# Optimization experiments

Measured on AMD Instinct MI355X. Metric: run time of the kernel, lower is better.

The kernel has to match this reference:

```python
import jax, jax.numpy as jnp
import numpy as np
from jax import lax

DN = ('NCDHW', 'OIDHW', 'NCDHW')
BN_EPS = 1e-5
COS_EPS = 1e-8   # torch CosineSimilarity eps
L1_EPS = 1e-12   # F.normalize default eps


def _lrelu(x):
    return jnp.where(x >= 0, x, 0.2 * x)


def _bn(x, g, b):
    # BatchNorm3d in training mode: batch statistics over (N, D, H, W)
    m = jnp.mean(x, axis=(0, 2, 3, 4), keepdims=True)
    v = jnp.var(x, axis=(0, 2, 3, 4), keepdims=True)
    return g[None, :, None, None, None] * (x - m) * lax.rsqrt(v + BN_EPS) + b[None, :, None, None, None]


def _conv(x, w, b, stride):
    y = lax.conv_general_dilated(x, w, window_strides=stride, padding=[(1, 1)] * 3,
                                 dimension_numbers=DN)
    return y + b[None, :, None, None, None]


def _convT(x, w, b, stride, out_pad):
    # ConvTranspose3d(k=3, padding=1, output_padding=out_pad) == input-dilated conv
    # with flipped kernel and padding (k-1-p, k-1-p+op) = (1, 1+op).
    k = jnp.flip(w, axis=(2, 3, 4))
    y = lax.conv_general_dilated(x, k, window_strides=(1, 1, 1),
                                 padding=[(1, 1 + o) for o in out_pad],
                                 lhs_dilation=stride, dimension_numbers=DN)
    return y + b[None, :, None, None, None]


def setup_inputs() -> dict:
    key = jax.random.key(0)
    ks = jax.random.split(key, 20)
    d = {}
    d['x'] = jax.random.normal(ks[0], (2, 1, 16, 256, 256), jnp.float32)
    enc = [(96, 1), (128, 96), (256, 128), (256, 256)]
    for i, (co, ci) in enumerate(enc):
        fan = ci * 27
        d[f'enc_w{i+1}'] = jax.random.normal(ks[1 + i], (co, ci, 3, 3, 3), jnp.float32) * np.float32(np.sqrt(2.0 / fan))
        d[f'enc_b{i+1}'] = jnp.zeros((co,), jnp.float32)
        d[f'enc_g{i+1}'] = jnp.ones((co,), jnp.float32)
        d[f'enc_be{i+1}'] = jnp.zeros((co,), jnp.float32)
    d['mem'] = jax.random.normal(ks[5], (2000, 256), jnp.float32) * np.float32(1.0 / np.sqrt(256))
    dec = [(256, 256), (128, 256), (96, 128), (1, 96)]  # (Cout, Cin)
    for i, (co, ci) in enumerate(dec):
        fan = ci * 27
        d[f'dec_w{i+1}'] = jax.random.normal(ks[6 + i], (co, ci, 3, 3, 3), jnp.float32) * np.float32(np.sqrt(2.0 / fan))
        d[f'dec_b{i+1}'] = jnp.zeros((co,), jnp.float32)
        if i < 3:
            d[f'dec_g{i+1}'] = jnp.ones((co,), jnp.float32)
            d[f'dec_be{i+1}'] = jnp.zeros((co,), jnp.float32)
    return d


def _forward(x,
             enc_w1, enc_b1, enc_g1, enc_be1,
             enc_w2, enc_b2, enc_g2, enc_be2,
             enc_w3, enc_b3, enc_g3, enc_be3,
             enc_w4, enc_b4, enc_g4, enc_be4,
             mem,
             dec_w1, dec_b1, dec_g1, dec_be1,
             dec_w2, dec_b2, dec_g2, dec_be2,
             dec_w3, dec_b3, dec_g3, dec_be3,
             dec_w4, dec_b4):
    # ---- encoder ----
    f = _lrelu(_bn(_conv(x, enc_w1, enc_b1, (1, 2, 2)), enc_g1, enc_be1))
    f = _lrelu(_bn(_conv(f, enc_w2, enc_b2, (2, 2, 2)), enc_g2, enc_be2))
    f = _lrelu(_bn(_conv(f, enc_w3, enc_b3, (2, 2, 2)), enc_g3, enc_be3))
    f = _lrelu(_bn(_conv(f, enc_w4, enc_b4, (2, 2, 2)), enc_g4, enc_be4))
    # ---- memory addressing (cosine similarity without materializing repeats) ----
    N, C, D, H, W = f.shape
    z = f.transpose(0, 2, 3, 4, 1).reshape(-1, C)                    # [M, C]
    z_norm = jnp.linalg.norm(z, axis=1, keepdims=True)               # [M, 1]
    m_norm = jnp.linalg.norm(mem, axis=1, keepdims=True)             # [K, 1]
    num = z @ mem.T                                                  # [M, K]
    den = jnp.maximum(z_norm * m_norm.T, COS_EPS)
    w = jax.nn.softmax(num / den, axis=1)
    w_hat = jax.nn.relu(w)
    w_hat = w_hat / jnp.maximum(jnp.sum(jnp.abs(w_hat), axis=1, keepdims=True), L1_EPS)
    z_hat = w_hat @ mem                                              # [M, C]
    zf = z_hat.reshape(N, D, H, W, C).transpose(0, 4, 1, 2, 3)
    # ---- decoder ----
    y = _lrelu(_bn(_convT(zf, dec_w1, dec_b1, (2, 2, 2), (1, 1, 1)), dec_g1, dec_be1))
    y = _lrelu(_bn(_convT(y, dec_w2, dec_b2, (2, 2, 2), (1, 1, 1)), dec_g2, dec_be2))
    y = _lrelu(_bn(_convT(y, dec_w3, dec_b3, (2, 2, 2), (1, 1, 1)), dec_g3, dec_be3))
    out = _convT(y, dec_w4, dec_b4, (1, 2, 2), (0, 1, 1))
    return out, w_hat


def reference(x,
              enc_w1, enc_b1, enc_g1, enc_be1,
              enc_w2, enc_b2, enc_g2, enc_be2,
              enc_w3, enc_b3, enc_g3, enc_be3,
              enc_w4, enc_b4, enc_g4, enc_be4,
              mem,
              dec_w1, dec_b1, dec_g1, dec_be1,
              dec_w2, dec_b2, dec_g2, dec_be2,
              dec_w3, dec_b3, dec_g3, dec_be3,
              dec_w4, dec_b4):
    return _forward(x,
                    enc_w1, enc_b1, enc_g1, enc_be1,
                    enc_w2, enc_b2, enc_g2, enc_be2,
                    enc_w3, enc_b3, enc_g3, enc_be3,
                    enc_w4, enc_b4, enc_g4, enc_be4,
                    mem,
                    dec_w1, dec_b1, dec_g1, dec_be1,
                    dec_w2, dec_b2, dec_g2, dec_be2,
                    dec_w3, dec_b3, dec_g3, dec_be3,
                    dec_w4, dec_b4)
```

## Files before the change

### kernel.cpp

```cpp
#include <hip/hip_runtime.h>
#include <math.h>

typedef unsigned short u16;
typedef __bf16 bf16;
typedef bf16 bf16x8 __attribute__((ext_vector_type(8)));
typedef float f32x4 __attribute__((ext_vector_type(4)));
typedef u16 u16x8 __attribute__((ext_vector_type(8)));

__device__ inline float b2f(u16 u){ unsigned x = ((unsigned)u) << 16; return __builtin_bit_cast(float, x); }
__device__ inline u16 f2b(float f){ bf16 b = (bf16)f; return __builtin_bit_cast(u16, b); }
__device__ inline f32x4 mfma16(bf16x8 a, bf16x8 b, f32x4 c){
    return __builtin_amdgcn_mfma_f32_16x16x32_bf16(a, b, c, 0, 0, 0);
}
__device__ inline void unp8(uint4 v, float* f){
    f[0]=__builtin_bit_cast(float, v.x<<16); f[1]=__builtin_bit_cast(float, v.x&0xffff0000u);
    f[2]=__builtin_bit_cast(float, v.y<<16); f[3]=__builtin_bit_cast(float, v.y&0xffff0000u);
    f[4]=__builtin_bit_cast(float, v.z<<16); f[5]=__builtin_bit_cast(float, v.z&0xffff0000u);
    f[6]=__builtin_bit_cast(float, v.w<<16); f[7]=__builtin_bit_cast(float, v.w&0xffff0000u);
}

struct Rep7 {
    const float* src[7];
    u16* dst[7];
    int co[7];
    int ci[7];
};
__global__ __launch_bounds__(256) void repack7_k(Rep7 a)
{
    int w = blockIdx.y;
    const float* src = a.src[w]; u16* dst = a.dst[w];
    int Co = a.co[w], Ci = a.ci[w];
    int tot = 27 * Co * Ci;
    for (int e = blockIdx.x * 256 + threadIdx.x; e < tot; e += gridDim.x * 256) {
        int ci = e % Ci; int t2 = e / Ci; int co = t2 % Co; int tp = t2 / Co;
        dst[e] = f2b(src[(size_t)(co * Ci + ci) * 27 + tp]);
    }
}

template<bool ISCONV, int CK, int BN>
__global__ __launch_bounds__(512) void conv_mfma3_k(
    const u16* __restrict__ in, const u16* __restrict__ wt,
    const float* __restrict__ bias, u16* __restrict__ out,
    float* __restrict__ pm, float* __restrict__ pv,
    int Ci, int Co, int Di, int Hi, int Wi,
    int ld, int lh, int lw, int Do, int Ho, int Wo)
{
    constexpr int NK = CK / 32;
    constexpr int NF = BN / 32;
    __shared__ u16 As[128][CK + 8];
    __shared__ u16 Bs[BN][CK + 8];
    const int tid = threadIdx.x;
    const int mtile = blockIdx.x, co0 = blockIdx.y * BN;
    int pd = 0, ph = 0, pw = 0;
    if (!ISCONV) { int bz = blockIdx.z; pd = bz >> 2; ph = (bz >> 1) & 1; pw = bz & 1; }

    const int arow = tid >> 2, seg = tid & 3;
    int xo, yo, zo, n;
    { int m = mtile * 128 + arow;
      xo = m & ((1 << lw) - 1); m >>= lw;
      yo = m & ((1 << lh) - 1); m >>= lh;
      zo = m & ((1 << ld) - 1); n = m >> ld; }
    const bool isb = arow < BN;

    const int wave = tid >> 6, lane = tid & 63;
    const int wm = wave >> 1, wn = wave & 1;
    const int fr = lane & 15, fs = lane >> 4;

    f32x4 acc[2][NF];
    #pragma unroll
    for (int mf = 0; mf < 2; ++mf)
        #pragma unroll
        for (int nf = 0; nf < NF; ++nf) acc[mf][nf] = f32x4{0,0,0,0};

    const int ntd = ISCONV ? 3 : pd + 1;
    const int nth = ISCONV ? 3 : ph + 1;
    const int ntw = ISCONV ? 3 : pw + 1;
    const size_t HiWi = (size_t)Hi * Wi;

    for (int jd = 0; jd < ntd; ++jd) {
        int zi = ISCONV ? 2 * zo + jd - 1 : zo + (pd ? jd : 0);
        int wd = ISCONV ? jd : (pd ? (jd ? 0 : 2) : 1);
        bool vz = (unsigned)zi < (unsigned)Di;
        for (int jh = 0; jh < nth; ++jh) {
            int yi = ISCONV ? 2 * yo + jh - 1 : yo + (ph ? jh : 0);
            int wh = ISCONV ? jh : (ph ? (jh ? 0 : 2) : 1);
            bool vy = vz && ((unsigned)yi < (unsigned)Hi);
            for (int jw = 0; jw < ntw; ++jw) {
                int xi = ISCONV ? 2 * xo + jw - 1 : xo + (pw ? jw : 0);
                int ww = ISCONV ? jw : (pw ? (jw ? 0 : 2) : 1);
                bool va = vy && ((unsigned)xi < (unsigned)Wi);
                size_t abase = 0;
                if (va) abase = (((size_t)(n * Di + zi)) * HiWi + (size_t)yi * Wi + xi) * Ci;
                int widx = wd * 9 + wh * 3 + ww;
                size_t bbase = ((size_t)widx * Co + (co0 + arow)) * (size_t)Ci;
                for (int ck = 0; ck < Ci; ck += CK) {
                    uint4 av[NK], bv[NK];
                    #pragma unroll
                    for (int k = 0; k < NK; ++k) {
                        int col = ck + k * 32 + seg * 8;
                        av[k] = va  ? *reinterpret_cast<const uint4*>(in + abase + col) : uint4{0,0,0,0};
                        bv[k] = isb ? *reinterpret_cast<const uint4*>(wt + bbase + col) : uint4{0,0,0,0};
                    }
                    __syncthreads();
                    #pragma unroll
                    for (int k = 0; k < NK; ++k) {
                        *reinterpret_cast<uint4*>(&As[arow][k * 32 + seg * 8]) = av[k];
                        if (isb) *reinterpret_cast<uint4*>(&Bs[arow][k * 32 + seg * 8]) = bv[k];
                    }
                    __syncthreads();
                    #pragma unroll
                    for (int k = 0; k < NK; ++k) {
                        bf16x8 a0 = *reinterpret_cast<const bf16x8*>(&As[wm * 32      + fr][k * 32 + fs * 8]);
                        bf16x8 a1 = *reinterpret_cast<const bf16x8*>(&As[wm * 32 + 16 + fr][k * 32 + fs * 8]);
                        #pragma unroll
                        for (int nf = 0; nf < NF; ++nf) {
                            bf16x8 b = *reinterpret_cast<const bf16x8*>(
                                &Bs[wn * (BN / 2) + nf * 16 + fr][k * 32 + fs * 8]);
                            acc[0][nf] = mfma16(a0, b, acc[0][nf]);
                            acc[1][nf] = mfma16(a1, b, acc[1][nf]);
                        }
                    }
                }
            }
        }
    }
    float bi[NF], s[NF], q[NF];
    #pragma unroll
    for (int nf = 0; nf < NF; ++nf) {
        bi[nf] = bias[co0 + wn * (BN / 2) + nf * 16 + fr];
        s[nf] = 0.f; q[nf] = 0.f;
    }
    #pragma unroll
    for (int mf = 0; mf < 2; ++mf) {
        #pragma unroll
        for (int j = 0; j < 4; ++j) {
            int rm = mtile * 128 + wm * 32 + mf * 16 + fs * 4 + j;
            size_t vox;
            if (ISCONV) vox = (size_t)rm;
            else {
                int X = rm & ((1 << lw) - 1); int m2 = rm >> lw;
                int Y = m2 & ((1 << lh) - 1); m2 >>= lh;
                int Z = m2 & ((1 << ld) - 1); int nn = m2 >> ld;
                vox = (((size_t)(nn * Do + (2 * Z + pd))) * Ho + (2 * Y + ph)) * Wo + (2 * X + pw);
            }
            #pragma unroll
            for (int nf = 0; nf < NF; ++nf) {
                float f = acc[mf][nf][j] + bi[nf];
                out[vox * Co + (co0 + wn * (BN / 2) + nf * 16 + fr)] = f2b(f);
                s[nf] += f; q[nf] += f * f;
            }
        }
    }
    __syncthreads();
    float* bnS = reinterpret_cast<float*>(&As[0][0]);
    float* bnQ = bnS + BN * 16;
    #pragma unroll
    for (int nf = 0; nf < NF; ++nf) {
        int cl = wn * (BN / 2) + nf * 16 + fr;
        bnS[cl * 16 + wm * 4 + fs] = s[nf];
        bnQ[cl * 16 + wm * 4 + fs] = q[nf];
    }
    __syncthreads();
    if (tid < BN) {
        float S = 0.f, Q = 0.f;
        #pragma unroll
        for (int i = 0; i < 16; ++i) { S += bnS[tid * 16 + i]; Q += bnQ[tid * 16 + i]; }
        int p = blockIdx.x + gridDim.x * (blockIdx.y + gridDim.y * blockIdx.z);
        pm[(size_t)p * BN + tid] = S;
        pv[(size_t)p * BN + tid] = Q;
    }
}

__global__ __launch_bounds__(256) void enc1_k(
    const float* __restrict__ x, const float* __restrict__ w,
    const float* __restrict__ bias, u16* __restrict__ out)
{
    __shared__ float Xi[4 * 17 * 33];
    __shared__ float Wl[96 * 27];
    __shared__ float Bl[96];
    const int tid = threadIdx.x;
    int t = blockIdx.x;
    const int tx = t & 7; t >>= 3;
    const int ty = t & 15; t >>= 4;
    const int tz = t;
    const int n = blockIdx.y;
    const int z0 = tz * 2, y0 = ty * 8, x0 = tx * 16;
    for (int i = tid; i < 2592; i += 256) Wl[i] = w[i];
    for (int i = tid; i < 96; i += 256) Bl[i] = bias[i];
    for (int i = tid; i < 2244; i += 256) {
        int fz = i / 561; int r = i - fz * 561; int fy = r / 33; int fx = r - fy * 33;
        int zi = z0 - 1 + fz, yi = 2 * y0 - 1 + fy, xi = 2 * x0 - 1 + fx;
        float v = 0.f;
        if ((unsigned)zi < 16u && (unsigned)yi < 256u && (unsigned)xi < 256u)
            v = x[((size_t)(n * 16 + zi) * 256 + yi) * 256 + xi];
        Xi[i] = v;
    }
    __syncthreads();
    const int lx = tid & 15, ly = (tid >> 4) & 7, lz = tid >> 7;
    float iv[27];
    #pragma unroll
    for (int kd = 0; kd < 3; ++kd)
        #pragma unroll
        for (int kh = 0; kh < 3; ++kh)
            #pragma unroll
            for (int kw = 0; kw < 3; ++kw)
                iv[kd * 9 + kh * 3 + kw] = Xi[(lz + kd) * 561 + (2 * ly + kh) * 33 + (2 * lx + kw)];
    size_t vox = ((size_t)(n * 16 + z0 + lz) * 128 + (y0 + ly)) * 128 + (x0 + lx);
    u16* op = out + vox * 96;
    #pragma unroll
    for (int og = 0; og < 12; ++og) {
        u16x8 pk;
        #pragma unroll
        for (int oo = 0; oo < 8; ++oo) {
            int o = og * 8 + oo;
            float a = Bl[o];
            #pragma unroll
            for (int tp = 0; tp < 27; ++tp) a += iv[tp] * Wl[o * 27 + tp];
            pk[oo] = f2b(a);
        }
        *reinterpret_cast<u16x8*>(op + og * 8) = pk;
    }
}

__global__ __launch_bounds__(256) void dec4g_k(
    const u16* __restrict__ in, const u16* __restrict__ wt4,
    float* __restrict__ P)
{
    __shared__ u16 As[64][120];
    __shared__ u16 Bs[32][120];
    const int tid = threadIdx.x;
    const int vox0 = blockIdx.x << 6;
    for (int i = tid; i < 384; i += 256) {
        int row = i / 12, seg = i - row * 12;
        uint4 v = {0,0,0,0};
        if (row < 27) v = *reinterpret_cast<const uint4*>(wt4 + row * 96 + seg * 8);
        *reinterpret_cast<uint4*>(&Bs[row][seg * 8]) = v;
    }
    for (int i = tid; i < 768; i += 256) {
        int row = i / 12, seg = i - row * 12;
        uint4 v = *reinterpret_cast<const uint4*>(in + (size_t)(vox0 + row) * 96 + seg * 8);
        *reinterpret_cast<uint4*>(&As[row][seg * 8]) = v;
    }
    __syncthreads();
    const int wave = tid >> 6, lane = tid & 63;
    const int fr = lane & 15, fs = lane >> 4;
    f32x4 acc0 = {0,0,0,0}, acc1 = {0,0,0,0};
    #pragma unroll
    for (int kk = 0; kk < 3; ++kk) {
        bf16x8 a  = *reinterpret_cast<const bf16x8*>(&As[wave * 16 + fr][kk * 32 + fs * 8]);
        bf16x8 b0 = *reinterpret_cast<const bf16x8*>(&Bs[fr     ][kk * 32 + fs * 8]);
        bf16x8 b1 = *reinterpret_cast<const bf16x8*>(&Bs[16 + fr][kk * 32 + fs * 8]);
        acc0 = mfma16(a, b0, acc0);
        acc1 = mfma16(a, b1, acc1);
    }
    #pragma unroll
    for (int j = 0; j < 4; ++j) {
        int vox = vox0 + wave * 16 + fs * 4 + j;
        P[(size_t)vox * 32 + fr]      = acc0[j];
        P[(size_t)vox * 32 + 16 + fr] = acc1[j];
    }
}

__global__ __launch_bounds__(256) void dec4s_k(
    const float* __restrict__ P, const float* __restrict__ bias,
    float* __restrict__ out)
{
    __shared__ float Pl[180 * 33];
    const int tid = threadIdx.x;
    int b = blockIdx.x;
    const int tx = b & 15; b >>= 4;
    const int ty = b & 31; b >>= 5;
    const int tz = b;
    const int n = blockIdx.y;
    const int Z0 = tz * 2, Y0 = ty * 8, X0 = tx * 16;
    const int yi0 = Y0 >> 1, xi0 = X0 >> 1;
    for (int i = tid; i < 5760; i += 256) {
        int row = i >> 5, c = i & 31;
        int dz = row / 45; int r = row - dz * 45; int dy = r / 9; int dx = r - dy * 9;
        int zi = Z0 - 1 + dz, yi = yi0 + dy, xi = xi0 + dx;
        float v = 0.f;
        if (zi >= 0 && zi < 16 && yi < 128 && xi < 128)
            v = P[((size_t)((n * 16 + zi) * 128 + yi) * 128 + xi) * 32 + c];
        Pl[row * 33 + c] = v;
    }
    __syncthreads();
    const int lx = tid & 15, ly = (tid >> 4) & 7, lz = tid >> 7;
    float acc = bias[0];
    #pragma unroll
    for (int qd = 0; qd < 3; ++qd) {
        int t = Z0 + lz + qd - 1;
        if (t < 0 || t >= 16) continue;
        int dz = lz + qd;
        #pragma unroll
        for (int qh = 0; qh < 3; ++qh) {
            int u = ly + qh - 1;
            if (u & 1) continue;
            int dy = u >> 1;
            #pragma unroll
            for (int qw = 0; qw < 3; ++qw) {
                int v = lx + qw - 1;
                if (v & 1) continue;
                int dx = v >> 1;
                int widx = (2 - qd) * 9 + (2 - qh) * 3 + (2 - qw);
                acc += Pl[(dz * 45 + dy * 9 + dx) * 33 + widx];
            }
        }
    }
    out[((size_t)(n * 16 + Z0 + lz) * 256 + (Y0 + ly)) * 256 + (X0 + lx)] = acc;
}

__global__ __launch_bounds__(256) void bnstat_k(
    const u16* __restrict__ a, float* __restrict__ pm, float* __restrict__ pv,
    int C, unsigned total8)
{
    __shared__ float sS[256][8];
    __shared__ float sQ[256][8];
    unsigned g = blockIdx.x * 256 + threadIdx.x;
    unsigned stride = gridDim.x * 256;
    float s[8] = {0,0,0,0,0,0,0,0}, q[8] = {0,0,0,0,0,0,0,0};
    for (unsigned i = g; i < total8; i += stride) {
        uint4 v = *reinterpret_cast<const uint4*>(a + (size_t)i * 8);
        float f[8]; unp8(v, f);
        #pragma unroll
        for (int e = 0; e < 8; ++e) { s[e] += f[e]; q[e] += f[e] * f[e]; }
    }
    #pragma unroll
    for (int e = 0; e < 8; ++e) { sS[threadIdx.x][e] = s[e]; sQ[threadIdx.x][e] = q[e]; }
    __syncthreads();
    int c = threadIdx.x;
    if (c < C) {
        int C8 = C >> 3;
        int B = (int)((blockIdx.x * 2048u) % (unsigned)C);
        int r = c - B; r %= C; if (r < 0) r += C;
        int e = r & 7, t0 = r >> 3;
        float S = 0.f, Q = 0.f;
        for (int tt = t0; tt < 256; tt += C8) { S += sS[tt][e]; Q += sQ[tt][e]; }
        pm[blockIdx.x * C + c] = S;
        pv[blockIdx.x * C + c] = Q;
    }
}

__global__ __launch_bounds__(64) void bnfin_k(
    const float* __restrict__ pm, const float* __restrict__ pv,
    const float* __restrict__ g, const float* __restrict__ be,
    float* __restrict__ sc, float* __restrict__ sb, int C, int G, float invcnt)
{
    int c = blockIdx.x;
    float S = 0.f, Q = 0.f;
    for (int b = threadIdx.x; b < G; b += 64) { S += pm[b * C + c]; Q += pv[b * C + c]; }
    #pragma unroll
    for (int off = 32; off; off >>= 1) {
        S += __shfl_down(S, off, 64);
        Q += __shfl_down(Q, off, 64);
    }
    if (threadIdx.x == 0) {
        float m = S * invcnt;
        float v = Q * invcnt - m * m;
        float s = g[c] * rsqrtf(v + 1e-5f);
        sc[c] = s; sb[c] = be[c] - m * s;
    }
}

__global__ __launch_bounds__(64) void bnfin3_k(
    const float* __restrict__ pm, const float* __restrict__ pv,
    const float* __restrict__ g, const float* __restrict__ be,
    float* __restrict__ sc, float* __restrict__ sb,
    int C, int BNl, int gx, int gy, int gz, float invcnt)
{
    int c = blockIdx.x;
    int cog = c / BNl, cl = c % BNl;
    int tot = gx * gz;
    float S = 0.f, Q = 0.f;
    for (int i = threadIdx.x; i < tot; i += 64) {
        int bx = i % gx, bz = i / gx;
        int p = bx + gx * (cog + gy * bz);
        S += pm[(size_t)p * BNl + cl];
        Q += pv[(size_t)p * BNl + cl];
    }
    #pragma unroll
    for (int off = 32; off; off >>= 1) {
        S += __shfl_down(S, off, 64);
        Q += __shfl_down(Q, off, 64);
    }
    if (threadIdx.x == 0) {
        float m = S * invcnt;
        float v = Q * invcnt - m * m;
        float s = g[c] * rsqrtf(v + 1e-5f);
        sc[c] = s; sb[c] = be[c] - m * s;
    }
}

__global__ __launch_bounds__(256) void bnapply_k(
    u16* __restrict__ a, const float* __restrict__ sc, const float* __restrict__ sb,
    int C, unsigned total8)
{
    unsigned g = blockIdx.x * 256 + threadIdx.x;
    unsigned stride = gridDim.x * 256;
    int c0 = (int)((g * 8u) % (unsigned)C);
    float lsc[8], lsb[8];
    #pragma unroll
    for (int e = 0; e < 8; ++e) { lsc[e] = sc[c0 + e]; lsb[e] = sb[c0 + e]; }
    for (unsigned i = g; i < total8; i += stride) {
        uint4 v = *reinterpret_cast<const uint4*>(a + (size_t)i * 8);
        float f[8]; unp8(v, f);
        u16x8 pk;
        #pragma unroll
        for (int e = 0; e < 8; ++e) {
            float y = f[e] * lsc[e] + lsb[e];
            y = y >= 0.f ? y : 0.2f * y;
            pk[e] = f2b(y);
        }
        *reinterpret_cast<u16x8*>(a + (size_t)i * 8) = pk;
    }
}

__global__ __launch_bounds__(256) void memprep_k(
    const float* __restrict__ mem, u16* __restrict__ memb, u16* __restrict__ memT,
    float* __restrict__ mnorm)
{
    int k = blockIdx.x, c = threadIdx.x;
    if (k >= 2000) { memT[(size_t)c * 2048 + k] = 0; return; }
    float v = mem[(size_t)k * 256 + c];
    u16 b = f2b(v);
    memb[(size_t)k * 256 + c] = b;
    memT[(size_t)c * 2048 + k] = b;
    float s = v * v;
    #pragma unroll
    for (int off = 32; off; off >>= 1) s += __shfl_down(s, off, 64);
    __shared__ float red[4];
    if ((c & 63) == 0) red[c >> 6] = s;
    __syncthreads();
    if (c == 0) mnorm[k] = sqrtf(red[0] + red[1] + red[2] + red[3]);
}

__global__ __launch_bounds__(64) void znorm_k(
    const u16* __restrict__ z, float* __restrict__ znorm)
{
    int m = blockIdx.x, l = threadIdx.x;
    ushort4 v = *reinterpret_cast<const ushort4*>(z + (size_t)m * 256 + l * 4);
    float a = b2f(v.x), b = b2f(v.y), cc = b2f(v.z), d = b2f(v.w);
    float s = a * a + b * b + cc * cc + d * d;
    #pragma unroll
    for (int off = 32; off; off >>= 1) s += __shfl_down(s, off, 64);
    if (l == 0) znorm[m] = sqrtf(s);
}

__global__ __launch_bounds__(256) void scores_mfma_k(
    const u16* __restrict__ z, const u16* __restrict__ memb,
    const float* __restrict__ znorm, const float* __restrict__ mnorm,
    float* __restrict__ scores)
{
    __shared__ u16 As[64][40];
    __shared__ u16 Bs[64][40];
    const int tid = threadIdx.x;
    const int m0 = blockIdx.x << 6, n0 = blockIdx.y << 6;
    const int arow = tid >> 2, seg = tid & 3;
    const bool bok = (n0 + arow) < 2000;
    const int wave = tid >> 6, lane = tid & 63;
    const int wm = wave >> 1, wn = wave & 1, fr = lane & 15, fs = lane >> 4;
    f32x4 acc00 = {0,0,0,0}, acc01 = {0,0,0,0}, acc10 = {0,0,0,0}, acc11 = {0,0,0,0};
    for (int k0 = 0; k0 < 256; k0 += 32) {
        uint4 avv = *reinterpret_cast<const uint4*>(z + (size_t)(m0 + arow) * 256 + k0 + seg * 8);
        uint4 bvv = {0,0,0,0};
        if (bok) bvv = *reinterpret_cast<const uint4*>(memb + (size_t)(n0 + arow) * 256 + k0 + seg * 8);
        __syncthreads();
        *reinterpret_cast<uint4*>(&As[arow][seg * 8]) = avv;
        *reinterpret_cast<uint4*>(&Bs[arow][seg * 8]) = bvv;
        __syncthreads();
        bf16x8 a0 = *reinterpret_cast<const bf16x8*>(&As[wm * 32      + fr][fs * 8]);
        bf16x8 a1 = *reinterpret_cast<const bf16x8*>(&As[wm * 32 + 16 + fr][fs * 8]);
        bf16x8 b0 = *reinterpret_cast<const bf16x8*>(&Bs[wn * 32      + fr][fs * 8]);
        bf16x8 b1 = *reinterpret_cast<const bf16x8*>(&Bs[wn * 32 + 16 + fr][fs * 8]);
        acc00 = mfma16(a0, b0, acc00);
        acc01 = mfma16(a0, b1, acc01);
        acc10 = mfma16(a1, b0, acc10);
        acc11 = mfma16(a1, b1, acc11);
    }
    const int c0 = n0 + wn * 32 + fr, c1 = c0 + 16;
    float mn0 = (c0 < 2000) ? mnorm[c0] : 1.f;
    float mn1 = (c1 < 2000) ? mnorm[c1] : 1.f;
    #pragma unroll
    for (int mi = 0; mi < 2; ++mi) {
        f32x4 aN0 = mi ? acc10 : acc00;
        f32x4 aN1 = mi ? acc11 : acc01;
        #pragma unroll
        for (int j = 0; j < 4; ++j) {
            int rm = m0 + wm * 32 + mi * 16 + fs * 4 + j;
            float zn = znorm[rm];
            if (c0 < 2000) scores[(size_t)rm * 2000 + c0] = aN0[j] / fmaxf(zn * mn0, 1e-8f);
            if (c1 < 2000) scores[(size_t)rm * 2000 + c1] = aN1[j] / fmaxf(zn * mn1, 1e-8f);
        }
    }
}

__global__ __launch_bounds__(256) void softmax2_k(
    float* __restrict__ w, u16* __restrict__ wb16)
{
    __shared__ float red[4];
    const int m = blockIdx.x, t = threadIdx.x;
    const bool act = t < 250;
    float v[8];
    if (act) {
        float4 p0 = *reinterpret_cast<const float4*>(w + (size_t)m * 2000 + t * 8);
        float4 p1 = *reinterpret_cast<const float4*>(w + (size_t)m * 2000 + t * 8 + 4);
        v[0]=p0.x; v[1]=p0.y; v[2]=p0.z; v[3]=p0.w;
        v[4]=p1.x; v[5]=p1.y; v[6]=p1.z; v[7]=p1.w;
    } else {
        for (int i = 0; i < 8; ++i) v[i] = -1e30f;
    }
    float mx = -1e30f;
    for (int i = 0; i < 8; ++i) mx = fmaxf(mx, v[i]);
    #pragma unroll
    for (int off = 32; off; off >>= 1) mx = fmaxf(mx, __shfl_down(mx, off, 64));
    if ((t & 63) == 0) red[t >> 6] = mx;
    __syncthreads();
    mx = fmaxf(fmaxf(red[0], red[1]), fmaxf(red[2], red[3]));
    __syncthreads();
    float e[8], sm = 0.f;
    for (int i = 0; i < 8; ++i) {
        e[i] = act ? expf(v[i] - mx) : 0.f;
        sm += e[i];
    }
    #pragma unroll
    for (int off = 32; off; off >>= 1) sm += __shfl_down(sm, off, 64);
    if ((t & 63) == 0) red[t >> 6] = sm;
    __syncthreads();
    float inv = 1.0f / (red[0] + red[1] + red[2] + red[3]);
    u16x8 pk = {0,0,0,0,0,0,0,0};
    if (act) {
        float r[8];
        for (int i = 0; i < 8; ++i) { r[i] = e[i] * inv; pk[i] = f2b(r[i]); }
        float4 o0, o1;
        o0.x=r[0]; o0.y=r[1]; o0.z=r[2]; o0.w=r[3];
        o1.x=r[4]; o1.y=r[5]; o1.z=r[6]; o1.w=r[7];
        *reinterpret_cast<float4*>(w + (size_t)m * 2000 + t * 8)     = o0;
        *reinterpret_cast<float4*>(w + (size_t)m * 2000 + t * 8 + 4) = o1;
    }
    *reinterpret_cast<u16x8*>(wb16 + (size_t)m * 2048 + t * 8) = pk;
}

__global__ __launch_bounds__(256) void zhat_mfma_k(
    const u16* __restrict__ wb16, const u16* __restrict__ memT,
    u16* __restrict__ zf)
{
    __shared__ u16 As[64][40];
    __shared__ u16 Bs[64][40];
    const int tid = threadIdx.x;
    const int m0 = blockIdx.x << 6, n0 = blockIdx.y << 6;
    const int arow = tid >> 2, seg = tid & 3;
    const int wave = tid >> 6, lane = tid & 63;
    const int wm = wave >> 1, wn = wave & 1, fr = lane & 15, fs = lane >> 4;
    f32x4 acc00 = {0,0,0,0}, acc01 = {0,0,0,0}, acc10 = {0,0,0,0}, acc11 = {0,0,0,0};
    for (int k0 = 0; k0 < 2048; k0 += 32) {
        uint4 avv = *reinterpret_cast<const uint4*>(wb16 + (size_t)(m0 + arow) * 2048 + k0 + seg * 8);
        uint4 bvv = *reinterpret_cast<const uint4*>(memT + (size_t)(n0 + arow) * 2048 + k0 + seg * 8);
        __syncthreads();
        *reinterpret_cast<uint4*>(&As[arow][seg * 8]) = avv;
        *reinterpret_cast<uint4*>(&Bs[arow][seg * 8]) = bvv;
        __syncthreads();
        bf16x8 a0 = *reinterpret_cast<const bf16x8*>(&As[wm * 32      + fr][fs * 8]);
        bf16x8 a1 = *reinterpret_cast<const bf16x8*>(&As[wm * 32 + 16 + fr][fs * 8]);
        bf16x8 b0 = *reinterpret_cast<const bf16x8*>(&Bs[wn * 32      + fr][fs * 8]);
        bf16x8 b1 = *reinterpret_cast<const bf16x8*>(&Bs[wn * 32 + 16 + fr][fs * 8]);
        acc00 = mfma16(a0, b0, acc00);
        acc01 = mfma16(a0, b1, acc01);
        acc10 = mfma16(a1, b0, acc10);
        acc11 = mfma16(a1, b1, acc11);
    }
    const int c0 = n0 + wn * 32 + fr, c1 = c0 + 16;
    #pragma unroll
    for (int mi = 0; mi < 2; ++mi) {
        f32x4 aN0 = mi ? acc10 : acc00;
        f32x4 aN1 = mi ? acc11 : acc01;
        #pragma unroll
        for (int j = 0; j < 4; ++j) {
            int rm = m0 + wm * 32 + mi * 16 + fs * 4 + j;
            zf[(size_t)rm * 256 + c0] = f2b(aN0[j]);
            zf[(size_t)rm * 256 + c1] = f2b(aN1[j]);
        }
    }
}

extern "C" void kernel_launch(void* const* d_in, const int* in_sizes, int n_in,
                              void* d_out, int out_size, void* d_ws, size_t ws_size,
                              hipStream_t stream)
{
    const float* x     = (const float*)d_in[0];
    const float* ew[4] = { (const float*)d_in[1],  (const float*)d_in[5],
                           (const float*)d_in[9],  (const float*)d_in[13] };
    const float* eb[4] = { (const float*)d_in[2],  (const float*)d_in[6],
                           (const float*)d_in[10], (const float*)d_in[14] };
    const float* eg[4] = { (const float*)d_in[3],  (const float*)d_in[7],
                           (const float*)d_in[11], (const float*)d_in[15] };
    const float* ebe[4]= { (const float*)d_in[4],  (const float*)d_in[8],
                           (const float*)d_in[12], (const float*)d_in[16] };
    const float* mem   = (const float*)d_in[17];
    const float* dw[4] = { (const float*)d_in[18], (const float*)d_in[22],
                           (const float*)d_in[26], (const float*)d_in[30] };
    const float* db[4] = { (const float*)d_in[19], (const float*)d_in[23],
                           (const float*)d_in[27], (const float*)d_in[31] };
    const float* dg[3] = { (const float*)d_in[20], (const float*)d_in[24],
                           (const float*)d_in[28] };
    const float* dbe[3]= { (const float*)d_in[21], (const float*)d_in[25],
                           (const float*)d_in[29] };

    float* outp  = (float*)d_out;
    float* w_out = (float*)d_out + 2097152;

    char* p = (char*)d_ws;
    auto take = [&](size_t bytes) -> char* {
        char* q = p; p += (bytes + 255) & ~(size_t)255; return q;
    };
    u16* b1   = (u16*)take(50331648ull * 2);
    u16* b2   = (u16*)take(8388608ull * 2);
    u16* b3   = (u16*)take(2097152ull * 2);
    u16* b4   = (u16*)take(262144ull * 2);
    u16* zf   = (u16*)take(262144ull * 2);
    u16* w2   = (u16*)take(331776ull * 2);
    u16* w3   = (u16*)take(884736ull * 2);
    u16* w4   = (u16*)take(1769472ull * 2);
    u16* wd1  = (u16*)take(1769472ull * 2);
    u16* wd2  = (u16*)take(884736ull * 2);
    u16* wd3  = (u16*)take(331776ull * 2);
    u16* wd4  = (u16*)take(2592ull * 2);
    u16* memb = (u16*)take(512000ull * 2);
    u16* memT = (u16*)take(524288ull * 2);
    u16* wb16 = (u16*)take(2097152ull * 2);
    float* P     = (float*)take(16777216ull * 4);
    float* pm    = (float*)take(1048576ull * 4);
    float* pv    = (float*)take(1048576ull * 4);
    float* scb   = (float*)take(512 * 4);
    float* mnorm = (float*)take(2048 * 4);
    float* znorm = (float*)take(1024 * 4);

    auto bnc = [&](u16* buf, const float* g, const float* be, int C, int BNl,
                   unsigned total8, int G, int gx, int gy, int gz) {
        bnfin3_k<<<C, 64, 0, stream>>>(pm, pv, g, be, scb, scb + 256,
                                       C, BNl, gx, gy, gz,
                                       (float)C / ((float)total8 * 8.0f));
        bnapply_k<<<G, 256, 0, stream>>>(buf, scb, scb + 256, C, total8);
    };

    Rep7 ra;
    ra.src[0]=ew[1]; ra.dst[0]=w2;  ra.co[0]=128; ra.ci[0]=96;
    ra.src[1]=ew[2]; ra.dst[1]=w3;  ra.co[1]=256; ra.ci[1]=128;
    ra.src[2]=ew[3]; ra.dst[2]=w4;  ra.co[2]=256; ra.ci[2]=256;
    ra.src[3]=dw[0]; ra.dst[3]=wd1; ra.co[3]=256; ra.ci[3]=256;
    ra.src[4]=dw[1]; ra.dst[4]=wd2; ra.co[4]=128; ra.ci[4]=256;
    ra.src[5]=dw[2]; ra.dst[5]=wd3; ra.co[5]=96;  ra.ci[5]=128;
    ra.src[6]=dw[3]; ra.dst[6]=wd4; ra.co[6]=1;   ra.ci[6]=96;
    repack7_k<<<dim3(64, 7), 256, 0, stream>>>(ra);
    memprep_k<<<2048, 256, 0, stream>>>(mem, memb, memT, mnorm);

    enc1_k<<<dim3(1024, 2), 256, 0, stream>>>(x, ew[0], eb[0], b1);
    bnstat_k<<<768, 256, 0, stream>>>(b1, pm, pv, 96, 6291456u);
    bnfin_k<<<96, 64, 0, stream>>>(pm, pv, eg[0], ebe[0], scb, scb + 256, 96, 768,
                                   96.0f / (6291456.0f * 8.0f));
    bnapply_k<<<768, 256, 0, stream>>>(b1, scb, scb + 256, 96, 6291456u);

    conv_mfma3_k<true, 96, 128><<<dim3(512, 1, 1), 512, 0, stream>>>(
        b1, w2, eb[1], b2, pm, pv, 96, 128, 16, 128, 128, 3, 6, 6, 8, 64, 64);
    bnc(b2, eg[1], ebe[1], 128, 128, 1048576u, 512, 512, 1, 1);

    conv_mfma3_k<true, 128, 64><<<dim3(64, 4, 1), 512, 0, stream>>>(
        b2, w3, eb[2], b3, pm, pv, 128, 256, 8, 64, 64, 2, 5, 5, 4, 32, 32);
    bnc(b3, eg[2], ebe[2], 256, 64, 262144u, 512, 64, 4, 1);

    conv_mfma3_k<true, 128, 64><<<dim3(8, 4, 1), 512, 0, stream>>>(
        b3, w4, eb[3], b4, pm, pv, 256, 256, 4, 32, 32, 1, 4, 4, 2, 16, 16);
    bnc(b4, eg[3], ebe[3], 256, 64, 32768u, 128, 8, 4, 1);

    znorm_k<<<1024, 64, 0, stream>>>(b4, znorm);
    scores_mfma_k<<<dim3(16, 32), 256, 0, stream>>>(b4, memb, znorm, mnorm, w_out);
    softmax2_k<<<1024, 256, 0, stream>>>(w_out, wb16);
    zhat_mfma_k<<<dim3(16, 4), 256, 0, stream>>>(wb16, memT, zf);

    conv_mfma3_k<false, 128, 64><<<dim3(8, 4, 8), 512, 0, stream>>>(
        zf, wd1, db[0], b3, pm, pv, 256, 256, 2, 16, 16, 1, 4, 4, 4, 32, 32);
    bnc(b3, dg[0], dbe[0], 256, 64, 262144u, 512, 8, 4, 8);

    conv_mfma3_k<false, 128, 64><<<dim3(64, 2, 8), 512, 0, stream>>>(
        b3, wd2, db[1], b2, pm, pv, 256, 128, 4, 32, 32, 2, 5, 5, 8, 64, 64);
    bnc(b2, dg[1], dbe[1], 128, 64, 1048576u, 512, 64, 2, 8);

    conv_mfma3_k<false, 128, 96><<<dim3(512, 1, 8), 512, 0, stream>>>(
        b2, wd3, db[2], b1, pm, pv, 128, 96, 8, 64, 64, 3, 6, 6, 16, 128, 128);
    bnc(b1, dg[2], dbe[2], 96, 96, 6291456u, 768, 512, 1, 8);

    dec4g_k<<<8192, 256, 0, stream>>>(b1, wd4, P);
    dec4s_k<<<dim3(4096, 2), 256, 0, stream>>>(P, db[3], outp);
}
```

Before: 779.8 us.

## Fuse final BN+LeakyReLU into dec4 GEMM load; stage enc1 output stores via LDS

```diff
diff --git a/kernel.cpp b/kernel.cpp
--- a/kernel.cpp
+++ b/kernel.cpp
@@ -175,9 +175,8 @@
     const float* __restrict__ x, const float* __restrict__ w,
     const float* __restrict__ bias, u16* __restrict__ out)
 {
-    __shared__ float Xi[4 * 17 * 33];
-    __shared__ float Wl[96 * 27];
-    __shared__ float Bl[96];
+    __shared__ uint4 smem[256 * 13];
+    float* Xi = reinterpret_cast<float*>(smem);
     const int tid = threadIdx.x;
     int t = blockIdx.x;
     const int tx = t & 7; t >>= 3;
@@ -185,8 +184,6 @@
     const int tz = t;
     const int n = blockIdx.y;
     const int z0 = tz * 2, y0 = ty * 8, x0 = tx * 16;
-    for (int i = tid; i < 2592; i += 256) Wl[i] = w[i];
-    for (int i = tid; i < 96; i += 256) Bl[i] = bias[i];
     for (int i = tid; i < 2244; i += 256) {
         int fz = i / 561; int r = i - fz * 561; int fy = r / 33; int fx = r - fy * 33;
         int zi = z0 - 1 + fz, yi = 2 * y0 - 1 + fy, xi = 2 * x0 - 1 + fx;
@@ -205,25 +202,36 @@
             #pragma unroll
             for (int kw = 0; kw < 3; ++kw)
                 iv[kd * 9 + kh * 3 + kw] = Xi[(lz + kd) * 561 + (2 * ly + kh) * 33 + (2 * lx + kw)];
-    size_t vox = ((size_t)(n * 16 + z0 + lz) * 128 + (y0 + ly)) * 128 + (x0 + lx);
-    u16* op = out + vox * 96;
+    __syncthreads();
     #pragma unroll
     for (int og = 0; og < 12; ++og) {
         u16x8 pk;
         #pragma unroll
         for (int oo = 0; oo < 8; ++oo) {
             int o = og * 8 + oo;
-            float a = Bl[o];
+            float a = bias[o];
             #pragma unroll
-            for (int tp = 0; tp < 27; ++tp) a += iv[tp] * Wl[o * 27 + tp];
+            for (int tp = 0; tp < 27; ++tp) a += iv[tp] * w[o * 27 + tp];
             pk[oo] = f2b(a);
         }
-        *reinterpret_cast<u16x8*>(op + og * 8) = pk;
+        smem[tid * 13 + og] = __builtin_bit_cast(uint4, pk);
+    }
+    __syncthreads();
+    #pragma unroll
+    for (int it = 0; it < 12; ++it) {
+        int i = it * 256 + tid;
+        int r = i / 192, j = i - r * 192;
+        int rz = r >> 3, ry = r & 7;
+        int v = r * 16 + j / 12, c8 = j % 12;
+        uint4 val = smem[v * 13 + c8];
+        size_t voxbase = ((size_t)(n * 16 + z0 + rz) * 128 + (y0 + ry)) * 128 + x0;
+        *reinterpret_cast<uint4*>(out + voxbase * 96 + (size_t)j * 8) = val;
     }
 }
 
 __global__ __launch_bounds__(256) void dec4g_k(
     const u16* __restrict__ in, const u16* __restrict__ wt4,
+    const float* __restrict__ sc, const float* __restrict__ sb,
     float* __restrict__ P)
 {
     __shared__ u16 As[64][120];
@@ -239,7 +247,16 @@
     for (int i = tid; i < 768; i += 256) {
         int row = i / 12, seg = i - row * 12;
         uint4 v = *reinterpret_cast<const uint4*>(in + (size_t)(vox0 + row) * 96 + seg * 8);
-        *reinterpret_cast<uint4*>(&As[row][seg * 8]) = v;
+        float f[8]; unp8(v, f);
+        int c0 = seg * 8;
+        u16x8 pk;
+        #pragma unroll
+        for (int e = 0; e < 8; ++e) {
+            float y = f[e] * sc[c0 + e] + sb[c0 + e];
+            y = y >= 0.f ? y : 0.2f * y;
+            pk[e] = f2b(y);
+        }
+        *reinterpret_cast<u16x8*>(&As[row][seg * 8]) = pk;
     }
     __syncthreads();
     const int wave = tid >> 6, lane = tid & 63;
@@ -634,11 +651,11 @@
     float* znorm = (float*)take(1024 * 4);
 
     auto bnc = [&](u16* buf, const float* g, const float* be, int C, int BNl,
-                   unsigned total8, int G, int gx, int gy, int gz) {
+                   unsigned total8, int G, int gx, int gy, int gz, bool apply) {
         bnfin3_k<<<C, 64, 0, stream>>>(pm, pv, g, be, scb, scb + 256,
                                        C, BNl, gx, gy, gz,
                                        (float)C / ((float)total8 * 8.0f));
-        bnapply_k<<<G, 256, 0, stream>>>(buf, scb, scb + 256, C, total8);
+        if (apply) bnapply_k<<<G, 256, 0, stream>>>(buf, scb, scb + 256, C, total8);
     };
 
     Rep7 ra;
@@ -660,15 +677,15 @@
 
     conv_mfma3_k<true, 96, 128><<<dim3(512, 1, 1), 512, 0, stream>>>(
         b1, w2, eb[1], b2, pm, pv, 96, 128, 16, 128, 128, 3, 6, 6, 8, 64, 64);
-    bnc(b2, eg[1], ebe[1], 128, 128, 1048576u, 512, 512, 1, 1);
+    bnc(b2, eg[1], ebe[1], 128, 128, 1048576u, 512, 512, 1, 1, true);
 
     conv_mfma3_k<true, 128, 64><<<dim3(64, 4, 1), 512, 0, stream>>>(
         b2, w3, eb[2], b3, pm, pv, 128, 256, 8, 64, 64, 2, 5, 5, 4, 32, 32);
-    bnc(b3, eg[2], ebe[2], 256, 64, 262144u, 512, 64, 4, 1);
+    bnc(b3, eg[2], ebe[2], 256, 64, 262144u, 512, 64, 4, 1, true);
 
     conv_mfma3_k<true, 128, 64><<<dim3(8, 4, 1), 512, 0, stream>>>(
         b3, w4, eb[3], b4, pm, pv, 256, 256, 4, 32, 32, 1, 4, 4, 2, 16, 16);
-    bnc(b4, eg[3], ebe[3], 256, 64, 32768u, 128, 8, 4, 1);
+    bnc(b4, eg[3], ebe[3], 256, 64, 32768u, 128, 8, 4, 1, true);
 
     znorm_k<<<1024, 64, 0, stream>>>(b4, znorm);
     scores_mfma_k<<<dim3(16, 32), 256, 0, stream>>>(b4, memb, znorm, mnorm, w_out);
@@ -677,16 +694,16 @@
 
     conv_mfma3_k<false, 128, 64><<<dim3(8, 4, 8), 512, 0, stream>>>(
         zf, wd1, db[0], b3, pm, pv, 256, 256, 2, 16, 16, 1, 4, 4, 4, 32, 32);
-    bnc(b3, dg[0], dbe[0], 256, 64, 262144u, 512, 8, 4, 8);
+    bnc(b3, dg[0], dbe[0], 256, 64, 262144u, 512, 8, 4, 8, true);
 
     conv_mfma3_k<false, 128, 64><<<dim3(64, 2, 8), 512, 0, stream>>>(
         b3, wd2, db[1], b2, pm, pv, 256, 128, 4, 32, 32, 2, 5, 5, 8, 64, 64);
-    bnc(b2, dg[1], dbe[1], 128, 64, 1048576u, 512, 64, 2, 8);
+    bnc(b2, dg[1], dbe[1], 128, 64, 1048576u, 512, 64, 2, 8, true);
 
     conv_mfma3_k<false, 128, 96><<<dim3(512, 1, 8), 512, 0, stream>>>(
         b2, wd3, db[2], b1, pm, pv, 128, 96, 8, 64, 64, 3, 6, 6, 16, 128, 128);
-    bnc(b1, dg[2], dbe[2], 96, 96, 6291456u, 768, 512, 1, 8);
-
-    dec4g_k<<<8192, 256, 0, stream>>>(b1, wd4, P);
+    bnc(b1, dg[2], dbe[2], 96, 96, 6291456u, 768, 512, 1, 8, false);
+
+    dec4g_k<<<8192, 256, 0, stream>>>(b1, wd4, scb, scb + 256, P);
     dec4s_k<<<dim3(4096, 2), 256, 0, stream>>>(P, db[3], outp);
 }
```

Result: faster. 706.5 us (-9.4%).
